# Optimization experiments

Measured on AMD Instinct MI355X. Metric: run time of the kernel, lower is better.

The kernel has to match this reference:

```python
import jax, jax.numpy as jnp
import numpy as np

B, S, H = 2, 2048, 4096
NUM_HEADS = 32
HEAD_DIM = H // NUM_HEADS
ROPE_BASE = 10000.0


def setup_inputs() -> dict:
    key = jax.random.key(0)
    k1, k2, k3 = jax.random.split(key, 3)
    hidden_states = jax.random.normal(k1, (B, S, H), dtype=jnp.float32)
    qkv_w = jax.random.normal(k2, (H, 3 * H), dtype=jnp.float32) * (H ** -0.5)
    o_w = jax.random.normal(k3, (H, H), dtype=jnp.float32) * (H ** -0.5)
    position_ids = jnp.broadcast_to(jnp.arange(S, dtype=jnp.int64), (B, S))
    return {"hidden_states": hidden_states, "qkv_w": qkv_w, "o_w": o_w,
            "position_ids": position_ids}


def _rope_tables(seq_len, dim, dtype):
    # LlamaRotaryEmbedding: inv_freq over even dims, emb = concat(freqs, freqs)
    inv_freq = 1.0 / (ROPE_BASE ** (jnp.arange(0, dim, 2, dtype=jnp.float32) / dim))
    t = jnp.arange(seq_len, dtype=jnp.float32)
    freqs = jnp.outer(t, inv_freq)              # [S, dim/2]
    emb = jnp.concatenate([freqs, freqs], -1)   # [S, dim]
    return jnp.cos(emb).astype(dtype), jnp.sin(emb).astype(dtype)


def _rotate_half(x):
    x1, x2 = jnp.split(x, 2, axis=-1)
    return jnp.concatenate([-x2, x1], axis=-1)


def reference(hidden_states, qkv_w, o_w, position_ids):
    b, q_len, h = hidden_states.shape
    nh, hd = NUM_HEADS, HEAD_DIM

    qkv = hidden_states @ qkv_w                 # [B, S, 3H]
    q, k, v = jnp.split(qkv, 3, axis=2)

    def shape(t):  # [B,S,H] -> [B, nh, S, hd]
        return t.reshape(b, q_len, nh, hd).transpose(0, 2, 1, 3)
    q, k, v = shape(q), shape(k), shape(v)

    cos_t, sin_t = _rope_tables(q_len, hd, hidden_states.dtype)
    cos = cos_t[position_ids][:, None, :, :]    # [B,1,S,hd]
    sin = sin_t[position_ids][:, None, :, :]
    q = q * cos + _rotate_half(q) * sin
    k = k * cos + _rotate_half(k) * sin

    # causal SDPA (past_key_value is None -> is_causal=True)
    scale = 1.0 / np.sqrt(hd)
    scores = jnp.einsum('bhqd,bhkd->bhqk', q, k) * scale
    causal = jnp.tril(jnp.ones((q_len, q_len), dtype=bool))
    scores = jnp.where(causal, scores, jnp.finfo(scores.dtype).min)
    attn = jax.nn.softmax(scores, axis=-1)
    ctx = jnp.einsum('bhqk,bhkd->bhqd', attn, v)

    out = ctx.transpose(0, 2, 1, 3).reshape(b, q_len, h) @ o_w
    return out
```

## Files before the change

kernel.cpp:

```cpp
#include <hip/hip_runtime.h>
#include <cstdint>
#include <cstddef>

using u16 = unsigned short;
using u32 = unsigned int;

typedef __bf16 bf16x8 __attribute__((ext_vector_type(8)));
typedef float f32x4 __attribute__((ext_vector_type(4)));

#define DEV static __device__ __forceinline__

DEV u16 f2bf(float f) {
  u32 u = __builtin_bit_cast(u32, f);
  u32 r = (u + 0x7fffu + ((u >> 16) & 1u)) >> 16;
  return (u16)r;
}
DEV float bf2f(u16 u) { return __builtin_bit_cast(float, ((u32)u) << 16); }

DEV void gload_lds16(const void* g, void* l) {
  __builtin_amdgcn_global_load_lds(
      (__attribute__((address_space(1))) void*)(void*)g,
      (__attribute__((address_space(3))) void*)l, 16, 0, 0);
}

__global__ __launch_bounds__(256) void k_f2bf(const float* __restrict__ in,
                                              u16* __restrict__ out, int n8) {
  int tid = blockIdx.x * 256 + threadIdx.x;
  int nt = gridDim.x * 256;
  for (int i = tid; i < n8; i += nt) {
    const float4* p = (const float4*)(in + (size_t)i * 8);
    float4 a = p[0], b = p[1];
    u32 w0 = (u32)f2bf(a.x) | ((u32)f2bf(a.y) << 16);
    u32 w1 = (u32)f2bf(a.z) | ((u32)f2bf(a.w) << 16);
    u32 w2 = (u32)f2bf(b.x) | ((u32)f2bf(b.y) << 16);
    u32 w3 = (u32)f2bf(b.z) | ((u32)f2bf(b.w) << 16);
    *(uint4*)(out + (size_t)i * 8) = make_uint4(w0, w1, w2, w3);
  }
}

__global__ __launch_bounds__(256) void k_convT(const float* __restrict__ W,
                                               u16* __restrict__ WT,
                                               int ncols, int krows) {
  __shared__ u16 tile[64 * 72];
  int r0 = blockIdx.x * 64, c0 = blockIdx.y * 64;
  int t = threadIdx.x;
#pragma unroll
  for (int i = 0; i < 4; ++i) {
    int slot = i * 256 + t;
    int r = slot >> 4, c = (slot & 15) * 4;
    float4 v = *(const float4*)(W + (size_t)(r0 + r) * ncols + c0 + c);
    tile[r * 72 + c] = f2bf(v.x);
    tile[r * 72 + c + 1] = f2bf(v.y);
    tile[r * 72 + c + 2] = f2bf(v.z);
    tile[r * 72 + c + 3] = f2bf(v.w);
  }
  __syncthreads();
#pragma unroll
  for (int i = 0; i < 2; ++i) {
    int slot = i * 256 + t;
    int c = slot >> 3, rr = (slot & 7) * 8;
    u32 w[4];
#pragma unroll
    for (int j = 0; j < 4; ++j) {
      u16 lo = tile[(rr + 2 * j) * 72 + c];
      u16 hi = tile[(rr + 2 * j + 1) * 72 + c];
      w[j] = (u32)lo | ((u32)hi << 16);
    }
    *(uint4*)(WT + (size_t)(c0 + c) * krows + r0 + rr) =
        make_uint4(w[0], w[1], w[2], w[3]);
  }
}

#define VM6 asm volatile("s_waitcnt vmcnt(6)" ::: "memory")
#define VM8 asm volatile("s_waitcnt vmcnt(8)" ::: "memory")
#define VM0 asm volatile("s_waitcnt vmcnt(0)" ::: "memory")

template <bool OUT_BF16>
__global__ __launch_bounds__(512, 2) void k_gemm256(const u16* __restrict__ A,
                                                    const u16* __restrict__ BT,
                                                    void* __restrict__ Cout,
                                                    int N, int K, int grid_m) {
  __shared__ __align__(16) u16 Asmem[2][16384];
  __shared__ __align__(16) u16 Bsmem[2][16384];
  const int nwg = gridDim.x;
  const int cpx = nwg >> 3;
  const int wg = (blockIdx.x & 7) * cpx + (blockIdx.x >> 3);
  const int row0 = (wg % grid_m) * 256;
  const int col0 = (wg / grid_m) * 256;
  const int tid = threadIdx.x;
  const int lane = tid & 63, wave = tid >> 6;
  const int wm = wave >> 2, wn = wave & 3;
  const int fr = lane & 15, fg = lane >> 4;
  const int NT = K >> 6;

  const int r_l0 = tid >> 3;
  const int gl = (tid & 7) ^ (r_l0 & 7);

#define STAGE_A(b, h, s)                                                          \
  do {                                                                            \
    const u16* src_ = A + (size_t)(row0 + (h)*128 + r_l0) * K + (s)*64 + gl * 8;  \
    gload_lds16(src_, &Asmem[b][(h)*8192 + tid * 8]);                             \
    gload_lds16(src_ + (size_t)64 * K, &Asmem[b][(h)*8192 + 4096 + tid * 8]);     \
  } while (0)
#define STAGE_B(b, h, s)                                                          \
  do {                                                                            \
    const u16* src_ = BT + (size_t)(col0 + (h)*128 + r_l0) * K + (s)*64 + gl * 8; \
    gload_lds16(src_, &Bsmem[b][(h)*8192 + tid * 8]);                             \
    gload_lds16(src_ + (size_t)64 * K, &Bsmem[b][(h)*8192 + 4096 + tid * 8]);     \
  } while (0)

  const int aBase = (wm * 64 + fr) * 64;
  const int bBase = (wn * 32 + fr) * 64;
  const int sg0 = ((fg) ^ (fr & 7)) * 8;
  const int sg1 = ((4 + fg) ^ (fr & 7)) * 8;
#define LDA(buf, mh, m, kk) \
  (*(const bf16x8*)(&Asmem[buf][aBase + (mh)*8192 + (m)*1024 + ((kk) ? sg1 : sg0)]))
#define LDB(buf, nh, n, kk) \
  (*(const bf16x8*)(&Bsmem[buf][bBase + (nh)*8192 + (n)*1024 + ((kk) ? sg1 : sg0)]))

  bf16x8 a[4][2], b0[2][2], b1[2][2];
  f32x4 acc[2][2][4][2] = {};

#define PHASE(buf, mh, nh, RDA, RDB, BP, STG, WT)                                  \
  {                                                                                \
    if (RDA) {                                                                     \
      _Pragma("unroll") for (int m_ = 0; m_ < 4; ++m_) {                           \
        a[m_][0] = LDA(buf, mh, m_, 0);                                            \
        a[m_][1] = LDA(buf, mh, m_, 1);                                            \
      }                                                                            \
    }                                                                              \
    if (RDB) {                                                                     \
      _Pragma("unroll") for (int n_ = 0; n_ < 2; ++n_) {                           \
        BP[n_][0] = LDB(buf, nh, n_, 0);                                           \
        BP[n_][1] = LDB(buf, nh, n_, 1);                                           \
      }                                                                            \
    }                                                                              \
    STG;                                                                           \
    __builtin_amdgcn_s_barrier();                                                  \
    __builtin_amdgcn_s_setprio(1);                                                 \
    _Pragma("unroll") for (int m_ = 0; m_ < 4; ++m_) {                             \
      _Pragma("unroll") for (int n_ = 0; n_ < 2; ++n_) {                           \
        acc[mh][nh][m_][n_] = __builtin_amdgcn_mfma_f32_16x16x32_bf16(             \
            a[m_][0], BP[n_][0], acc[mh][nh][m_][n_], 0, 0, 0);                    \
        acc[mh][nh][m_][n_] = __builtin_amdgcn_mfma_f32_16x16x32_bf16(             \
            a[m_][1], BP[n_][1], acc[mh][nh][m_][n_], 0, 0, 0);                    \
      }                                                                            \
    }                                                                              \
    __builtin_amdgcn_s_setprio(0);                                                 \
    WT;                                                                            \
    __builtin_amdgcn_s_barrier();                                                  \
  }

  STAGE_A(0, 0, 0); STAGE_B(0, 0, 0);
  STAGE_A(0, 1, 0); STAGE_B(0, 1, 0);
  STAGE_A(1, 0, 1); STAGE_B(1, 0, 1);
  VM8;
  __builtin_amdgcn_s_barrier();

  const int nIt = NT >> 1;
  for (int it = 0; it < nIt; ++it) {
    const int T = 2 * it;
    const int s2 = (T + 2 < NT) ? T + 2 : T;
    const int s3 = (T + 3 < NT) ? T + 3 : T;
    PHASE(0, 0, 0, true,  true,  b0, { STAGE_A(1, 1, T + 1); }, VM6);
    PHASE(0, 0, 1, false, true,  b1, { STAGE_B(1, 1, T + 1); }, ((void)0));
    PHASE(0, 1, 0, true,  false, b0, { STAGE_A(0, 0, s2); },    ((void)0));
    PHASE(0, 1, 1, false, false, b1, { STAGE_B(0, 0, s2); },    VM8);
    PHASE(1, 0, 0, true,  true,  b0, { STAGE_A(0, 1, s2); },    VM6);
    PHASE(1, 0, 1, false, true,  b1, { STAGE_B(0, 1, s2); },    ((void)0));
    PHASE(1, 1, 0, true,  false, b0, { STAGE_A(1, 0, s3); },    ((void)0));
    PHASE(1, 1, 1, false, false, b1, { STAGE_B(1, 0, s3); },    VM8);
  }
  VM0;

#pragma unroll
  for (int mh = 0; mh < 2; ++mh)
#pragma unroll
    for (int nh = 0; nh < 2; ++nh)
#pragma unroll
      for (int m = 0; m < 4; ++m) {
        const int growb = row0 + mh * 128 + wm * 64 + m * 16 + fg * 4;
#pragma unroll
        for (int rr = 0; rr < 4; ++rr) {
#pragma unroll
          for (int n = 0; n < 2; ++n) {
            const int gcol = col0 + nh * 128 + wn * 32 + n * 16 + fr;
            if (OUT_BF16)
              ((u16*)Cout)[(size_t)(growb + rr) * N + gcol] = f2bf(acc[mh][nh][m][n][rr]);
            else
              ((float*)Cout)[(size_t)(growb + rr) * N + gcol] = acc[mh][nh][m][n][rr];
          }
        }
      }
#undef PHASE
#undef LDA
#undef LDB
#undef STAGE_A
#undef STAGE_B
}

__global__ __launch_bounds__(256) void k_rope(const u16* __restrict__ qkv,
                                              u16* __restrict__ Qh,
                                              u16* __restrict__ Kh) {
  const int row = blockIdx.x;
  const int s = row & 2047;
  const int b = row >> 11;
  const int t = threadIdx.x;
  __shared__ float cs[64], sn[64];
  if (t < 64) {
    float inv = powf(10000.0f, -(float)t * (1.0f / 64.0f));
    float ang = (float)s * inv;
    cs[t] = cosf(ang);
    sn[t] = sinf(ang);
  }
  __syncthreads();
  const float qscale = 0.08838834764831845f;
#pragma unroll
  for (int i = 0; i < 8; ++i) {
    int idx = i * 256 + t;
    int h = idx >> 6, dh = idx & 63;
    float c = cs[dh], sv = sn[dh];
    size_t base = (size_t)row * 12288 + h * 128 + dh;
    size_t obase = ((size_t)(b * 32 + h) * 2048 + s) * 128 + dh;
    float q1 = bf2f(qkv[base]), q2 = bf2f(qkv[base + 64]);
    Qh[obase] = f2bf((q1 * c - q2 * sv) * qscale);
    Qh[obase + 64] = f2bf((q2 * c + q1 * sv) * qscale);
    float k1 = bf2f(qkv[base + 4096]), k2 = bf2f(qkv[base + 4096 + 64]);
    Kh[obase] = f2bf(k1 * c - k2 * sv);
    Kh[obase + 64] = f2bf(k2 * c + k1 * sv);
  }
}

__global__ __launch_bounds__(256) void k_vtrans(const u16* __restrict__ qkv,
                                                u16* __restrict__ VTh) {
  __shared__ u16 tile[64 * 136];
  const int hb = blockIdx.x;
  const int st = blockIdx.y;
  const int b = hb >> 5, h = hb & 31;
  const int t = threadIdx.x;
#pragma unroll
  for (int i = 0; i < 4; ++i) {
    int slot = i * 256 + t;
    int r = slot >> 4, c = (slot & 15) * 8;
    *(uint4*)(tile + r * 136 + c) =
        *(const uint4*)(qkv + (size_t)(b * 2048 + st * 64 + r) * 12288 + 8192 + h * 128 + c);
  }
  __syncthreads();
#pragma unroll
  for (int i = 0; i < 4; ++i) {
    int slot = i * 256 + t;
    int d = slot >> 3, c2 = (slot & 7) * 8;
    u32 w[4];
#pragma unroll
    for (int j = 0; j < 4; ++j) {
      u16 lo = tile[(c2 + 2 * j) * 136 + d];
      u16 hi = tile[(c2 + 2 * j + 1) * 136 + d];
      w[j] = (u32)lo | ((u32)hi << 16);
    }
    *(uint4*)(VTh + ((size_t)hb * 128 + d) * 2048 + st * 64 + c2) =
        make_uint4(w[0], w[1], w[2], w[3]);
  }
}

__global__ __launch_bounds__(256, 2) void k_attn(const u16* __restrict__ Qh,
                                                 const u16* __restrict__ Kh,
                                                 const u16* __restrict__ VTh,
                                                 u16* __restrict__ CTX) {
  __shared__ __align__(16) u16 smem[8704 + 9216 + 4 * 2304];
  u16* Klds = smem;
  u16* Vlds = smem + 8704;
  const int qt = blockIdx.x;
  const int hb = blockIdx.y;
  const int tid = threadIdx.x;
  const int lane = tid & 63, wave = tid >> 6;
  const int fr = lane & 15, fg = lane >> 4;
  u16* Plds = smem + 8704 + 9216 + wave * 2304;
  const int qbase = qt * 128;
  const int wq0 = qbase + wave * 32;
  const size_t hOff = (size_t)hb * 2048 * 128;

  bf16x8 qf[2][4];
#pragma unroll
  for (int qb = 0; qb < 2; ++qb)
#pragma unroll
    for (int ks = 0; ks < 4; ++ks)
      qf[qb][ks] =
          *(const bf16x8*)(Qh + hOff + (size_t)(wq0 + qb * 16 + fr) * 128 + ks * 32 + fg * 8);

  f32x4 o[8][2] = {};
  float m[2] = {-1e30f, -1e30f}, lsum[2] = {0.f, 0.f};
  const int jend = 2 * (qt + 1);
  const int jmask = wq0 >> 6;

  for (int j = 0; j < jend; ++j) {
    __syncthreads();
#pragma unroll
    for (int i = 0; i < 4; ++i) {
      int slot = i * 256 + tid;
      int r = slot >> 4, c = (slot & 15) * 8;
      *(uint4*)(Klds + r * 136 + c) =
          *(const uint4*)(Kh + hOff + (size_t)(j * 64 + r) * 128 + c);
    }
#pragma unroll
    for (int i = 0; i < 4; ++i) {
      int slot = i * 256 + tid;
      int d = slot >> 3, c = (slot & 7) * 8;
      *(uint4*)(Vlds + d * 72 + c) =
          *(const uint4*)(VTh + hOff + (size_t)d * 2048 + j * 64 + c);
    }
    __syncthreads();

    f32x4 st[4][2] = {};
#pragma unroll
    for (int ks = 0; ks < 4; ++ks) {
#pragma unroll
      for (int f = 0; f < 4; ++f) {
        bf16x8 kf = *(const bf16x8*)(Klds + (f * 16 + fr) * 136 + ks * 32 + fg * 8);
#pragma unroll
        for (int qb = 0; qb < 2; ++qb)
          st[f][qb] = __builtin_amdgcn_mfma_f32_16x16x32_bf16(kf, qf[qb][ks], st[f][qb], 0, 0, 0);
      }
    }
    if (j >= jmask) {
#pragma unroll
      for (int f = 0; f < 4; ++f)
#pragma unroll
        for (int qb = 0; qb < 2; ++qb)
#pragma unroll
          for (int r = 0; r < 4; ++r) {
            int kv = j * 64 + f * 16 + fg * 4 + r;
            int q = wq0 + qb * 16 + fr;
            if (kv > q) st[f][qb][r] = -1e30f;
          }
    }
#pragma unroll
    for (int qb = 0; qb < 2; ++qb) {
      float pmax = -1e30f;
#pragma unroll
      for (int f = 0; f < 4; ++f)
#pragma unroll
        for (int r = 0; r < 4; ++r) pmax = fmaxf(pmax, st[f][qb][r]);
      pmax = fmaxf(pmax, __shfl_xor(pmax, 16));
      pmax = fmaxf(pmax, __shfl_xor(pmax, 32));
      float mnew = fmaxf(m[qb], pmax);
      float factor = __expf(m[qb] - mnew);
      float psum = 0.f;
#pragma unroll
      for (int f = 0; f < 4; ++f) {
        float p0 = __expf(st[f][qb][0] - mnew);
        float p1 = __expf(st[f][qb][1] - mnew);
        float p2 = __expf(st[f][qb][2] - mnew);
        float p3 = __expf(st[f][qb][3] - mnew);
        psum += (p0 + p1) + (p2 + p3);
        u32 w0 = (u32)f2bf(p0) | ((u32)f2bf(p1) << 16);
        u32 w1 = (u32)f2bf(p2) | ((u32)f2bf(p3) << 16);
        *(uint2*)(Plds + (qb * 16 + fr) * 72 + f * 16 + fg * 4) = make_uint2(w0, w1);
      }
      psum += __shfl_xor(psum, 16);
      psum += __shfl_xor(psum, 32);
      lsum[qb] = lsum[qb] * factor + psum;
      m[qb] = mnew;
#pragma unroll
      for (int db = 0; db < 8; ++db) o[db][qb] *= factor;
    }
#pragma unroll
    for (int ks2 = 0; ks2 < 2; ++ks2) {
      bf16x8 pf[2];
#pragma unroll
      for (int qb = 0; qb < 2; ++qb)
        pf[qb] = *(const bf16x8*)(Plds + (qb * 16 + fr) * 72 + ks2 * 32 + fg * 8);
#pragma unroll
      for (int db = 0; db < 8; ++db) {
        bf16x8 vf = *(const bf16x8*)(Vlds + (db * 16 + fr) * 72 + ks2 * 32 + fg * 8);
#pragma unroll
        for (int qb = 0; qb < 2; ++qb)
          o[db][qb] = __builtin_amdgcn_mfma_f32_16x16x32_bf16(vf, pf[qb], o[db][qb], 0, 0, 0);
      }
    }
  }

  float inv[2] = {1.f / lsum[0], 1.f / lsum[1]};
  __syncthreads();
  u16* cst = smem + wave * 32 * 136;
#pragma unroll
  for (int db = 0; db < 8; ++db)
#pragma unroll
    for (int qb = 0; qb < 2; ++qb) {
      u32 w0 = (u32)f2bf(o[db][qb][0] * inv[qb]) | ((u32)f2bf(o[db][qb][1] * inv[qb]) << 16);
      u32 w1 = (u32)f2bf(o[db][qb][2] * inv[qb]) | ((u32)f2bf(o[db][qb][3] * inv[qb]) << 16);
      *(uint2*)(cst + (qb * 16 + fr) * 136 + db * 16 + fg * 4) = make_uint2(w0, w1);
    }
  __syncthreads();
  const int b = hb >> 5, h = hb & 31;
#pragma unroll
  for (int i = 0; i < 8; ++i) {
    int slot = i * 256 + tid;
    int qr = slot >> 4, c = (slot & 15) * 8;
    *(uint4*)(CTX + (size_t)(b * 2048 + qbase + qr) * 4096 + h * 128 + c) =
        *(const uint4*)(smem + qr * 136 + c);
  }
}

extern "C" void kernel_launch(void* const* d_in, const int* in_sizes, int n_in,
                              void* d_out, int out_size, void* d_ws, size_t ws_size,
                              hipStream_t stream) {
  const float* hidden = (const float*)d_in[0];
  const float* qkv_w = (const float*)d_in[1];
  const float* o_w = (const float*)d_in[2];
  float* out = (float*)d_out;
  if (ws_size < (256ull << 20)) return;
  char* ws = (char*)d_ws;
  u16* Xb    = (u16*)(ws + 0);
  u16* WqkvT = (u16*)(ws + (32ull << 20));
  u16* QKV   = (u16*)(ws + (128ull << 20));
  u16* VTh   = (u16*)(ws + (224ull << 20));
  u16* Qh    = (u16*)(ws + (32ull << 20));
  u16* Kh    = (u16*)(ws + (64ull << 20));
  u16* WoT   = (u16*)(ws + (96ull << 20));
  u16* CTX   = (u16*)(ws + 0);

  k_f2bf<<<2048, 256, 0, stream>>>(hidden, Xb, 16777216 / 8);
  k_convT<<<dim3(64, 192), 256, 0, stream>>>(qkv_w, WqkvT, 12288, 4096);
  k_gemm256<true><<<768, 512, 0, stream>>>(Xb, WqkvT, QKV, 12288, 4096, 16);
  k_rope<<<4096, 256, 0, stream>>>(QKV, Qh, Kh);
  k_vtrans<<<dim3(64, 32), 256, 0, stream>>>(QKV, VTh);
  k_convT<<<dim3(64, 64), 256, 0, stream>>>(o_w, WoT, 4096, 4096);
  k_attn<<<dim3(16, 64), 256, 0, stream>>>(Qh, Kh, VTh, CTX);
  k_gemm256<false><<<256, 512, 0, stream>>>(CTX, WoT, out, 4096, 4096, 16);
}
```

Measured before the change: 788.6 us.

## Swizzled direct-to-LDS attention loads, lazy softmax rescale, reversed tile order, precomputed RoPE table

In the attention kernel, K and V^T tiles now go straight from global memory into LDS through global_load_lds, using an XOR swizzle instead of padded rows to avoid bank conflicts. The kernel also raises wave priority around the MFMA sections and skips the online-softmax rescale unless the running max grows by more than 8. The grid is reordered so heads vary fastest and the longest causal query tiles are launched first. RoPE now reads a cos/sin table built once by a new k_trig kernel and processes 8 elements per thread with 16-byte loads and stores. The lazy-rescale threshold lets exponentials reach up to e^8 before rescaling, which adds some numerical risk in bf16 P.

```diff
diff --git a/kernel.cpp b/kernel.cpp
--- a/kernel.cpp
+++ b/kernel.cpp
@@ -199,7 +199,16 @@
 #undef STAGE_B
 }
 
+__global__ __launch_bounds__(128) void k_trig(float* __restrict__ T) {
+  const int s = blockIdx.x;
+  const int t = threadIdx.x;
+  float inv = powf(10000.0f, -(float)(t & 63) * (1.0f / 64.0f));
+  float ang = (float)s * inv;
+  T[(size_t)s * 128 + t] = (t < 64) ? cosf(ang) : sinf(ang);
+}
+
 __global__ __launch_bounds__(256) void k_rope(const u16* __restrict__ qkv,
+                                              const float* __restrict__ T,
                                               u16* __restrict__ Qh,
                                               u16* __restrict__ Kh) {
   const int row = blockIdx.x;
@@ -207,27 +216,35 @@
   const int b = row >> 11;
   const int t = threadIdx.x;
   __shared__ float cs[64], sn[64];
-  if (t < 64) {
-    float inv = powf(10000.0f, -(float)t * (1.0f / 64.0f));
-    float ang = (float)s * inv;
-    cs[t] = cosf(ang);
-    sn[t] = sinf(ang);
+  if (t < 128) {
+    float v = T[(size_t)s * 128 + t];
+    if (t < 64) cs[t] = v; else sn[t - 64] = v;
   }
   __syncthreads();
+  const int h = t >> 3, seg = t & 7;
   const float qscale = 0.08838834764831845f;
-#pragma unroll
-  for (int i = 0; i < 8; ++i) {
-    int idx = i * 256 + t;
-    int h = idx >> 6, dh = idx & 63;
-    float c = cs[dh], sv = sn[dh];
-    size_t base = (size_t)row * 12288 + h * 128 + dh;
-    size_t obase = ((size_t)(b * 32 + h) * 2048 + s) * 128 + dh;
-    float q1 = bf2f(qkv[base]), q2 = bf2f(qkv[base + 64]);
-    Qh[obase] = f2bf((q1 * c - q2 * sv) * qscale);
-    Qh[obase + 64] = f2bf((q2 * c + q1 * sv) * qscale);
-    float k1 = bf2f(qkv[base + 4096]), k2 = bf2f(qkv[base + 4096 + 64]);
-    Kh[obase] = f2bf(k1 * c - k2 * sv);
-    Kh[obase + 64] = f2bf(k2 * c + k1 * sv);
+  const size_t base = (size_t)row * 12288 + h * 128 + seg * 8;
+  const size_t obase = ((size_t)(b * 32 + h) * 2048 + s) * 128 + seg * 8;
+
+#pragma unroll
+  for (int mat = 0; mat < 2; ++mat) {
+    const u16* src = qkv + base + mat * 4096;
+    u16* dst = (mat == 0 ? Qh : Kh);
+    const float sc = (mat == 0) ? qscale : 1.0f;
+    uint4 lo = *(const uint4*)(src);
+    uint4 hi = *(const uint4*)(src + 64);
+    const u16* x1 = (const u16*)&lo;
+    const u16* x2 = (const u16*)&hi;
+    u16 o1[8], o2[8];
+#pragma unroll
+    for (int k = 0; k < 8; ++k) {
+      float c = cs[seg * 8 + k], sv = sn[seg * 8 + k];
+      float a = bf2f(x1[k]), d = bf2f(x2[k]);
+      o1[k] = f2bf((a * c - d * sv) * sc);
+      o2[k] = f2bf((d * c + a * sv) * sc);
+    }
+    *(uint4*)(dst + obase) = *(const uint4*)o1;
+    *(uint4*)(dst + obase + 64) = *(const uint4*)o2;
   }
 }
 
@@ -266,15 +283,15 @@
                                                  const u16* __restrict__ Kh,
                                                  const u16* __restrict__ VTh,
                                                  u16* __restrict__ CTX) {
-  __shared__ __align__(16) u16 smem[8704 + 9216 + 4 * 2304];
+  __shared__ __align__(16) u16 smem[8192 + 8192 + 4 * 2304];
   u16* Klds = smem;
-  u16* Vlds = smem + 8704;
-  const int qt = blockIdx.x;
-  const int hb = blockIdx.y;
+  u16* Vlds = smem + 8192;
+  const int hb = blockIdx.x;
+  const int qt = 15 - blockIdx.y;
   const int tid = threadIdx.x;
   const int lane = tid & 63, wave = tid >> 6;
   const int fr = lane & 15, fg = lane >> 4;
-  u16* Plds = smem + 8704 + 9216 + wave * 2304;
+  u16* Plds = smem + 16384 + wave * 2304;
   const int qbase = qt * 128;
   const int wq0 = qbase + wave * 32;
   const size_t hOff = (size_t)hb * 2048 * 128;
@@ -292,35 +309,41 @@
   const int jend = 2 * (qt + 1);
   const int jmask = wq0 >> 6;
 
+  const int krow_ = tid >> 4, kg_ = tid & 15;
+  const int vrow_ = tid >> 3, vg_ = tid & 7;
+
   for (int j = 0; j < jend; ++j) {
     __syncthreads();
 #pragma unroll
     for (int i = 0; i < 4; ++i) {
-      int slot = i * 256 + tid;
-      int r = slot >> 4, c = (slot & 15) * 8;
-      *(uint4*)(Klds + r * 136 + c) =
-          *(const uint4*)(Kh + hOff + (size_t)(j * 64 + r) * 128 + c);
+      int row = i * 16 + krow_;
+      int gs = kg_ ^ (row & 7);
+      gload_lds16(Kh + hOff + (size_t)(j * 64 + row) * 128 + gs * 8,
+                  Klds + (i * 256 + tid) * 8);
     }
 #pragma unroll
     for (int i = 0; i < 4; ++i) {
-      int slot = i * 256 + tid;
-      int d = slot >> 3, c = (slot & 7) * 8;
-      *(uint4*)(Vlds + d * 72 + c) =
-          *(const uint4*)(VTh + hOff + (size_t)d * 2048 + j * 64 + c);
+      int row = i * 32 + vrow_;
+      int gs = vg_ ^ (row & 7);
+      gload_lds16(VTh + hOff + (size_t)row * 2048 + j * 64 + gs * 8,
+                  Vlds + (i * 256 + tid) * 8);
     }
     __syncthreads();
 
     f32x4 st[4][2] = {};
+    __builtin_amdgcn_s_setprio(1);
 #pragma unroll
     for (int ks = 0; ks < 4; ++ks) {
 #pragma unroll
       for (int f = 0; f < 4; ++f) {
-        bf16x8 kf = *(const bf16x8*)(Klds + (f * 16 + fr) * 136 + ks * 32 + fg * 8);
+        bf16x8 kf = *(const bf16x8*)(Klds + (f * 16 + fr) * 128 +
+                                     (((ks * 4 + fg) ^ (fr & 7)) * 8));
 #pragma unroll
         for (int qb = 0; qb < 2; ++qb)
           st[f][qb] = __builtin_amdgcn_mfma_f32_16x16x32_bf16(kf, qf[qb][ks], st[f][qb], 0, 0, 0);
       }
     }
+    __builtin_amdgcn_s_setprio(0);
     if (j >= jmask) {
 #pragma unroll
       for (int f = 0; f < 4; ++f)
@@ -342,15 +365,21 @@
         for (int r = 0; r < 4; ++r) pmax = fmaxf(pmax, st[f][qb][r]);
       pmax = fmaxf(pmax, __shfl_xor(pmax, 16));
       pmax = fmaxf(pmax, __shfl_xor(pmax, 32));
-      float mnew = fmaxf(m[qb], pmax);
-      float factor = __expf(m[qb] - mnew);
+      if (!__all(pmax <= m[qb] + 8.0f)) {
+        float mnew = fmaxf(m[qb], pmax);
+        float factor = __expf(m[qb] - mnew);
+        lsum[qb] *= factor;
+#pragma unroll
+        for (int db = 0; db < 8; ++db) o[db][qb] *= factor;
+        m[qb] = mnew;
+      }
       float psum = 0.f;
 #pragma unroll
       for (int f = 0; f < 4; ++f) {
-        float p0 = __expf(st[f][qb][0] - mnew);
-        float p1 = __expf(st[f][qb][1] - mnew);
-        float p2 = __expf(st[f][qb][2] - mnew);
-        float p3 = __expf(st[f][qb][3] - mnew);
+        float p0 = __expf(st[f][qb][0] - m[qb]);
+        float p1 = __expf(st[f][qb][1] - m[qb]);
+        float p2 = __expf(st[f][qb][2] - m[qb]);
+        float p3 = __expf(st[f][qb][3] - m[qb]);
         psum += (p0 + p1) + (p2 + p3);
         u32 w0 = (u32)f2bf(p0) | ((u32)f2bf(p1) << 16);
         u32 w1 = (u32)f2bf(p2) | ((u32)f2bf(p3) << 16);
@@ -358,11 +387,9 @@
       }
       psum += __shfl_xor(psum, 16);
       psum += __shfl_xor(psum, 32);
-      lsum[qb] = lsum[qb] * factor + psum;
-      m[qb] = mnew;
-#pragma unroll
-      for (int db = 0; db < 8; ++db) o[db][qb] *= factor;
-    }
+      lsum[qb] += psum;
+    }
+    __builtin_amdgcn_s_setprio(1);
 #pragma unroll
     for (int ks2 = 0; ks2 < 2; ++ks2) {
       bf16x8 pf[2];
@@ -371,12 +398,14 @@
         pf[qb] = *(const bf16x8*)(Plds + (qb * 16 + fr) * 72 + ks2 * 32 + fg * 8);
 #pragma unroll
       for (int db = 0; db < 8; ++db) {
-        bf16x8 vf = *(const bf16x8*)(Vlds + (db * 16 + fr) * 72 + ks2 * 32 + fg * 8);
+        bf16x8 vf = *(const bf16x8*)(Vlds + (db * 16 + fr) * 64 +
+                                     (((ks2 * 4 + fg) ^ (fr & 7)) * 8));
 #pragma unroll
         for (int qb = 0; qb < 2; ++qb)
           o[db][qb] = __builtin_amdgcn_mfma_f32_16x16x32_bf16(vf, pf[qb], o[db][qb], 0, 0, 0);
       }
     }
+    __builtin_amdgcn_s_setprio(0);
   }
 
   float inv[2] = {1.f / lsum[0], 1.f / lsum[1]};
@@ -417,14 +446,16 @@
   u16* Qh    = (u16*)(ws + (32ull << 20));
   u16* Kh    = (u16*)(ws + (64ull << 20));
   u16* WoT   = (u16*)(ws + (96ull << 20));
+  float* Trig = (float*)(ws + (224ull << 20));
   u16* CTX   = (u16*)(ws + 0);
 
+  k_trig<<<2048, 128, 0, stream>>>(Trig);
   k_f2bf<<<2048, 256, 0, stream>>>(hidden, Xb, 16777216 / 8);
   k_convT<<<dim3(64, 192), 256, 0, stream>>>(qkv_w, WqkvT, 12288, 4096);
   k_gemm256<true><<<768, 512, 0, stream>>>(Xb, WqkvT, QKV, 12288, 4096, 16);
-  k_rope<<<4096, 256, 0, stream>>>(QKV, Qh, Kh);
+  k_rope<<<4096, 256, 0, stream>>>(QKV, Trig, Qh, Kh);
   k_vtrans<<<dim3(64, 32), 256, 0, stream>>>(QKV, VTh);
   k_convT<<<dim3(64, 64), 256, 0, stream>>>(o_w, WoT, 4096, 4096);
-  k_attn<<<dim3(16, 64), 256, 0, stream>>>(Qh, Kh, VTh, CTX);
+  k_attn<<<dim3(64, 16), 256, 0, stream>>>(Qh, Kh, VTh, CTX);
   k_gemm256<false><<<256, 512, 0, stream>>>(CTX, WoT, out, 4096, 4096, 16);
 }
```

Result: faster. 695.6 us (-11.8%).
